# Performance work log

Hardware: AMD Instinct MI355X
Metric: run time of the kernel (lower is better)

## Reference

```python
import jax, jax.numpy as jnp
import numpy as np

N, T, F_IN = 20000, 6, 64   # nodes, seq_len, in_channels
E = 320000                  # edges (avg degree 16)
H, C = 4, 64                # gat1 heads, hidden_channels


def setup_inputs() -> dict:
    key = jax.random.key(0)
    ks = jax.random.split(key, 16)
    p = lambda i, shape, s=0.1: jax.random.normal(ks[i], shape, jnp.float32) * s
    return dict(
        x=p(0, (N, T, F_IN), 1.0),
        edge_index=jax.random.randint(ks[1], (2, E), 0, N),
        # GATv2 layer 1: in=F_IN, out=C per head, H heads, concat
        Wl1=p(2, (F_IN, H * C)), Wr1=p(3, (F_IN, H * C)), att1=p(4, (H, C)), b1=jnp.zeros((H * C,), jnp.float32),
        # GATv2 layer 2: in=H*C, out=C, 1 head, no concat
        Wl2=p(5, (H * C, C)), Wr2=p(6, (H * C, C)), att2=p(7, (1, C)), b2=jnp.zeros((C,), jnp.float32),
        # LSTM (input C, hidden C), pytorch gate order i,f,g,o
        Wih=p(8, (4 * C, C)), Whh=p(9, (4 * C, C)), bih=jnp.zeros((4 * C,), jnp.float32), bhh=jnp.zeros((4 * C,), jnp.float32),
        # MLP head
        Wfc1=p(10, (C, C // 2)), bfc1=jnp.zeros((C // 2,), jnp.float32),
        Wout=p(11, (C // 2, 1)), bout=jnp.zeros((1,), jnp.float32),
    )


def gatv2(xt, src, dst, Wl, Wr, att, bias, n):
    """GATv2Conv (eval mode, no edge_attr): gather -> attn -> segment-softmax -> scatter."""
    heads = att.shape[0]
    d = Wl.shape[1] // heads
    xl = (xt @ Wl).reshape(n, heads, d)   # source transform
    xr = (xt @ Wr).reshape(n, heads, d)   # target transform
    e = jax.nn.leaky_relu(xl[src] + xr[dst], 0.2)           # [E, heads, d]
    logit = jnp.einsum('ehc,hc->eh', e, att)                # [E, heads]
    m = jax.ops.segment_max(logit, dst, num_segments=n)      # per-target max
    ex = jnp.exp(logit - m[dst])
    denom = jax.ops.segment_sum(ex, dst, num_segments=n)
    alpha = ex / denom[dst]                                  # segment softmax
    out = jax.ops.segment_sum(alpha[:, :, None] * xl[src], dst, num_segments=n)
    return out.reshape(n, heads * d) + bias


def reference(x, edge_index, Wl1, Wr1, att1, b1, Wl2, Wr2, att2, b2,
              Wih, Whh, bih, bhh, Wfc1, bfc1, Wout, bout):
    src, dst = edge_index[0], edge_index[1]
    n = x.shape[0]

    def gat_step(carry, xt):                    # per-timestep spatial encoder
        h1 = jax.nn.elu(gatv2(xt, src, dst, Wl1, Wr1, att1, b1, n))
        h2 = jax.nn.elu(gatv2(h1, src, dst, Wl2, Wr2, att2, b2, n))
        return carry, h2

    _, seq = jax.lax.scan(gat_step, 0.0, jnp.swapaxes(x, 0, 1))  # [T, N, C]

    hid = Whh.shape[1]

    def lstm_step(carry, xt):
        h, c = carry
        g = xt @ Wih.T + bih + h @ Whh.T + bhh
        i, f, gg, o = jnp.split(g, 4, axis=-1)
        c = jax.nn.sigmoid(f) * c + jax.nn.sigmoid(i) * jnp.tanh(gg)
        h = jax.nn.sigmoid(o) * jnp.tanh(c)
        return (h, c), None

    h0 = jnp.zeros((n, hid), x.dtype)
    (h_last, _), _ = jax.lax.scan(lstm_step, (h0, h0), seq)

    z = jax.nn.relu(h_last @ Wfc1 + bfc1)
    return z @ Wout + bout
```

## Files before the change

kernel.cpp:

```cpp
#include <hip/hip_runtime.h>
#include <hip/hip_fp16.h>
#include <math.h>

#define N_NODES 20000
#define T_STEPS 6
#define F_INCH  64
#define HC      256
#define CH      64

typedef _Float16 h8    __attribute__((ext_vector_type(8)));
typedef _Float16 hv2   __attribute__((ext_vector_type(2)));
typedef float    f32x4 __attribute__((ext_vector_type(4)));

__device__ __forceinline__ float fast_tanh(float x){
  float e = __expf(2.f*x);
  return 1.f - 2.f/(e + 1.f);
}

__device__ __forceinline__ float fdot2v(hv2 a, hv2 b, float c){
#if __has_builtin(__builtin_amdgcn_fdot2)
  return __builtin_amdgcn_fdot2(a, b, c, false);
#else
  return fmaf((float)a[0], (float)b[0], fmaf((float)a[1], (float)b[1], c));
#endif
}

__device__ __forceinline__ hv2 leaky2(hv2 t){
  hv2 s = t * (_Float16)0.2f;
#if __has_builtin(__builtin_elementwise_max)
  return __builtin_elementwise_max(t, s);
#else
  hv2 r;
  r[0] = (t[0] > s[0]) ? t[0] : s[0];
  r[1] = (t[1] > s[1]) ? t[1] : s[1];
  return r;
#endif
}

__global__ void k_count(const int* __restrict__ dst, int E, int* __restrict__ deg){
  int e = blockIdx.x*256 + threadIdx.x;
  if (e < E) atomicAdd(&deg[dst[e]], 1);
}

__global__ void k_scan(const int* __restrict__ deg, int* __restrict__ row_start, int N){
  __shared__ int wsum[16];
  const int PT = 20;
  int tid = threadIdx.x, wid = tid >> 6, lane = tid & 63;
  int base = tid*PT;
  int loc[PT];
  int s = 0;
  #pragma unroll
  for (int j = 0; j < PT; j++){
    int i = base + j;
    int v = (i < N) ? deg[i] : 0;
    loc[j] = s;
    s += v;
  }
  int ss = s;
  #pragma unroll
  for (int off = 1; off < 64; off <<= 1){
    int t = __shfl_up(ss, off, 64);
    if (lane >= off) ss += t;
  }
  if (lane == 63) wsum[wid] = ss;
  __syncthreads();
  if (tid < 16){
    int w = wsum[tid];
    #pragma unroll
    for (int off = 1; off < 16; off <<= 1){
      int t = __shfl_up(w, off, 64);
      if (tid >= off) w += t;
    }
    wsum[tid] = w;
  }
  __syncthreads();
  int pre = ((wid ? wsum[wid-1] : 0)) + (ss - s);
  #pragma unroll
  for (int j = 0; j < PT; j++){
    int i = base + j;
    if (i < N) row_start[i] = pre + loc[j];
  }
  if (tid == 0) row_start[N] = wsum[15];
}

__global__ void k_scatter(const int* __restrict__ src, const int* __restrict__ dst, int E,
                          const int* __restrict__ row_start, int* __restrict__ cursor,
                          int* __restrict__ csr){
  int e = blockIdx.x*256 + threadIdx.x;
  if (e < E){
    int d = dst[e];
    int pos = atomicAdd(&cursor[d], 1);
    csr[row_start[d] + pos] = src[e];
  }
}

__global__ void k_sort(const int* __restrict__ row_start, int* __restrict__ csr, int N){
  int wid = threadIdx.x >> 6, lane = threadIdx.x & 63;
  int d = blockIdx.x*4 + wid;
  if (d >= N) return;
  int s = row_start[d], e = row_start[d+1], len = e - s;
  if (len <= 1) return;
  if (len <= 64){
    int v = (lane < len) ? csr[s + lane] : 0x7fffffff;
    int rank = 0;
    for (int j = 0; j < len; j++){
      int vj = __shfl(v, j, 64);
      rank += (int)((vj < v) | ((vj == v) & (j < lane)));
    }
    if (lane < len) csr[s + rank] = v;
  } else if (lane == 0){
    for (int i = s+1; i < e; i++){
      int key = csr[i]; int j = i-1;
      while (j >= s && csr[j] > key){ csr[j+1] = csr[j]; j--; }
      csr[j+1] = key;
    }
  }
}

__device__ __forceinline__ void packB_dev(const float* __restrict__ B, _Float16* __restrict__ Bf,
                                          int K, int N, int idx){
  if (idx >= K*N) return;
  int j    = idx & 7;
  int lane = (idx >> 3) & 63;
  int ntk  = idx >> 9;
  int NT = N >> 4;
  int ks = ntk / NT, nt = ntk - ks*NT;
  int k = ks*32 + ((lane >> 4) << 3) + j;
  int n = nt*16 + (lane & 15);
  Bf[idx] = (_Float16)B[k*N + n];
}

__global__ void k_packall(const float* __restrict__ Wih, const float* __restrict__ Whh,
                          const float* __restrict__ bih, const float* __restrict__ bhh,
                          float* __restrict__ Wih4, float* __restrict__ Whh4,
                          float* __restrict__ biasc,
                          const float* __restrict__ Wl1, _Float16* __restrict__ Bl1f,
                          const float* __restrict__ Wr1, _Float16* __restrict__ Br1f,
                          const float* __restrict__ Wl2, _Float16* __restrict__ Bl2f,
                          const float* __restrict__ Wr2, _Float16* __restrict__ Br2f){
  int grp = blockIdx.x >> 6;
  int idx = (blockIdx.x & 63)*256 + threadIdx.x;
  if (grp == 0){
    if (idx < 64*256){
      int k = idx >> 8, cu = idx & 255;
      int u = cu >> 2, g = cu & 3;
      Wih4[idx] = Wih[(g*64+u)*64 + k];
      Whh4[idx] = Whh[(g*64+u)*64 + k];
    }
    if (idx < 256){
      int u = idx >> 2, g = idx & 3;
      biasc[idx] = bih[g*64+u] + bhh[g*64+u];
    }
  } else if (grp == 1){
    packB_dev(Wl1, Bl1f, 64, 256, idx);
  } else if (grp == 2){
    packB_dev(Wr1, Br1f, 64, 256, idx);
  } else if (grp == 3){
    packB_dev(Wl2, Bl2f, 256, 64, idx);
  } else {
    packB_dev(Wr2, Br2f, 256, 64, idx);
  }
}

__global__ __launch_bounds__(256) void k_gemm1_all(
    const float* __restrict__ x, const _Float16* __restrict__ B1f,
    const _Float16* __restrict__ B2f,
    __half* __restrict__ xl_all, __half* __restrict__ xr_all, int M){
  __shared__ _Float16 aT[32*72];
  int t = blockIdx.y;
  const float* A = x + t*F_INCH;
  _Float16* C1 = (_Float16*)(void*)xl_all + (size_t)t*N_NODES*HC;
  _Float16* C2 = (_Float16*)(void*)xr_all + (size_t)t*N_NODES*HC;
  int tid = threadIdx.x;
  int r0 = blockIdx.x*32;
  for (int i = tid; i < 32*64; i += 256){
    int r = i >> 6, k = i & 63;
    int row = r0 + r;
    aT[r*72 + k] = (row < M) ? (_Float16)A[(size_t)row*(T_STEPS*F_INCH) + k] : (_Float16)0.f;
  }
  __syncthreads();
  int wave = tid >> 6, lane = tid & 63;
  int m = wave & 1;
  const h8* Bfrag = (const h8*)((wave >> 1) ? B2f : B1f);
  _Float16* C = (wave >> 1) ? C2 : C1;
  int arow = m*16 + (lane & 15);
  int kb = (lane >> 4) * 8;
  h8 a0 = *(const h8*)&aT[arow*72 + kb];
  h8 a1 = *(const h8*)&aT[arow*72 + 32 + kb];
  f32x4 z = {0.f, 0.f, 0.f, 0.f};
  f32x4 acc[16];
  #pragma unroll
  for (int nt = 0; nt < 16; nt++) acc[nt] = z;
  #pragma unroll
  for (int nt = 0; nt < 16; nt++){
    h8 b0 = Bfrag[nt*64 + lane];
    h8 b1 = Bfrag[(16 + nt)*64 + lane];
    acc[nt] = __builtin_amdgcn_mfma_f32_16x16x32_f16(a0, b0, acc[nt], 0, 0, 0);
    acc[nt] = __builtin_amdgcn_mfma_f32_16x16x32_f16(a1, b1, acc[nt], 0, 0, 0);
  }
  int ccol = lane & 15, crow = (lane >> 4) * 4;
  #pragma unroll
  for (int nt = 0; nt < 16; nt++){
    #pragma unroll
    for (int r = 0; r < 4; r++){
      int row = r0 + m*16 + crow + r;
      if (row < M) C[(size_t)row*256 + nt*16 + ccol] = (_Float16)acc[nt][r];
    }
  }
}

__global__ __launch_bounds__(256) void k_gemm2_all(
    const __half* __restrict__ Aall, const _Float16* __restrict__ B1f,
    const _Float16* __restrict__ B2f,
    __half* __restrict__ C1h_all, __half* __restrict__ C2h_all, int M){
  __shared__ _Float16 aT[32*264];
  int t = blockIdx.y;
  const _Float16* A = (const _Float16*)(const void*)Aall + (size_t)t*N_NODES*HC;
  _Float16* C1 = (_Float16*)(void*)C1h_all + (size_t)t*N_NODES*CH;
  _Float16* C2 = (_Float16*)(void*)C2h_all + (size_t)t*N_NODES*CH;
  int tid = threadIdx.x;
  int r0 = blockIdx.x*32;
  h8 zh = {(_Float16)0.f,(_Float16)0.f,(_Float16)0.f,(_Float16)0.f,
           (_Float16)0.f,(_Float16)0.f,(_Float16)0.f,(_Float16)0.f};
  for (int i = tid; i < 32*32; i += 256){
    int r = i >> 5, c = i & 31;
    int row = r0 + r;
    h8 v = zh;
    if (row < M) v = *(const h8*)&A[(size_t)row*256 + c*8];
    *(h8*)&aT[r*264 + c*8] = v;
  }
  __syncthreads();
  int wave = tid >> 6, lane = tid & 63;
  int m = wave & 1;
  const h8* Bfrag = (const h8*)((wave >> 1) ? B2f : B1f);
  _Float16* C = (wave >> 1) ? C2 : C1;
  int arow = m*16 + (lane & 15);
  int kb = (lane >> 4) * 8;
  f32x4 z = {0.f, 0.f, 0.f, 0.f};
  f32x4 acc[4];
  #pragma unroll
  for (int nt = 0; nt < 4; nt++) acc[nt] = z;
  #pragma unroll
  for (int ks = 0; ks < 8; ks++){
    h8 a = *(const h8*)&aT[arow*264 + ks*32 + kb];
    #pragma unroll
    for (int nt = 0; nt < 4; nt++){
      h8 b = Bfrag[(ks*4 + nt)*64 + lane];
      acc[nt] = __builtin_amdgcn_mfma_f32_16x16x32_f16(a, b, acc[nt], 0, 0, 0);
    }
  }
  int ccol = lane & 15, crow = (lane >> 4) * 4;
  #pragma unroll
  for (int nt = 0; nt < 4; nt++){
    #pragma unroll
    for (int r = 0; r < 4; r++){
      int row = r0 + m*16 + crow + r;
      if (row < M) C[(size_t)row*64 + nt*16 + ccol] = (_Float16)acc[nt][r];
    }
  }
}

__global__ void k_gat1_all(const __half* __restrict__ xl_all, const __half* __restrict__ xr_all,
                           const int* __restrict__ row_start, const int* __restrict__ csr,
                           const float* __restrict__ att, const float* __restrict__ bias,
                           __half* __restrict__ out_all, int N){
  int wid = threadIdx.x >> 6, lane = threadIdx.x & 63;
  int dst = blockIdx.x*4 + wid;
  if (dst >= N) return;
  int t = blockIdx.y;
  const char* xlb = (const char*)(xl_all + (size_t)t*N_NODES*HC);
  const uint2* xrh = (const uint2*)(xr_all + (size_t)t*N_NODES*HC);
  uint2* outh = (uint2*)(out_all + (size_t)t*N_NODES*HC);
  uint2 xr_raw = xrh[(unsigned)(dst*64 + lane)];
  hv2 xr01 = *reinterpret_cast<hv2*>(&xr_raw.x);
  hv2 xr23 = *reinterpret_cast<hv2*>(&xr_raw.y);
  float4 at4 = ((const float4*)att)[lane];
  hv2 at01; at01[0] = (_Float16)at4.x; at01[1] = (_Float16)at4.y;
  hv2 at23; at23[0] = (_Float16)at4.z; at23[1] = (_Float16)at4.w;
  unsigned loff = lane*8u;
  int s0 = __builtin_amdgcn_readfirstlane(row_start[dst]);
  int s1 = __builtin_amdgcn_readfirstlane(row_start[dst+1]);
  float den = 0.f, ax = 0.f, ay = 0.f, az = 0.f, aw = 0.f;

  auto STEP = [&](uint2 raw){
    hv2 h01 = *reinterpret_cast<hv2*>(&raw.x);
    hv2 h23 = *reinterpret_cast<hv2*>(&raw.y);
    hv2 l01 = leaky2(h01 + xr01);
    hv2 l23 = leaky2(h23 + xr23);
    float p = fdot2v(l01, at01, fdot2v(l23, at23, 0.f));
    p += __shfl_xor(p, 1, 64);
    p += __shfl_xor(p, 2, 64);
    p += __shfl_xor(p, 4, 64);
    p += __shfl_xor(p, 8, 64);
    float w = __expf(p);
    den += w;
    ax = fmaf(w, (float)h01[0], ax);
    ay = fmaf(w, (float)h01[1], ay);
    az = fmaf(w, (float)h23[0], az);
    aw = fmaf(w, (float)h23[1], aw);
  };

  for (int base = s0; base < s1; base += 64){
    int rem = s1 - base;
    int cnt = rem < 64 ? rem : 64;
    int idxv = (base + lane < s1) ? csr[base + lane] : 0;
    auto LD = [&](int i)->uint2 {
      int s = __builtin_amdgcn_readlane(idxv, i & 63);
      return *(const uint2*)(xlb + (((size_t)(unsigned)s) << 9) + loff);
    };
    uint2 p0=LD(0), p1=LD(1), p2=LD(2), p3=LD(3);
    uint2 p4=LD(4), p5=LD(5), p6=LD(6), p7=LD(7);
    for (int i = 0; i < cnt; i += 4){
      uint2 n0=LD(i+8), n1=LD(i+9), n2=LD(i+10), n3=LD(i+11);
      if (i + 4 <= cnt){
        STEP(p0); STEP(p1); STEP(p2); STEP(p3);
      } else {
        STEP(p0);
        if (i+1 < cnt) STEP(p1);
        if (i+2 < cnt) STEP(p2);
        if (i+3 < cnt) STEP(p3);
      }
      p0=p4; p1=p5; p2=p6; p3=p7;
      p4=n0; p5=n1; p6=n2; p7=n3;
    }
  }
  float invd = (s1 > s0) ? 1.f/den : 0.f;
  float4 b4 = ((const float4*)bias)[lane];
  float rx = fmaf(ax, invd, b4.x);
  float ry = fmaf(ay, invd, b4.y);
  float rz = fmaf(az, invd, b4.z);
  float rw = fmaf(aw, invd, b4.w);
  rx = rx > 0.f ? rx : (__expf(rx) - 1.f);
  ry = ry > 0.f ? ry : (__expf(ry) - 1.f);
  rz = rz > 0.f ? rz : (__expf(rz) - 1.f);
  rw = rw > 0.f ? rw : (__expf(rw) - 1.f);
  __half2 o01 = __floats2half2_rn(rx, ry);
  __half2 o23 = __floats2half2_rn(rz, rw);
  uint2 o;
  o.x = *reinterpret_cast<unsigned int*>(&o01);
  o.y = *reinterpret_cast<unsigned int*>(&o23);
  outh[(unsigned)(dst*64 + lane)] = o;
}

__global__ void k_gat2_all(const __half* __restrict__ xl_all, const __half* __restrict__ xr_all,
                           const int* __restrict__ row_start, const int* __restrict__ csr,
                           const float* __restrict__ att, const float* __restrict__ bias,
                           __half* __restrict__ out_all, int N){
  int wid = threadIdx.x >> 6, lane = threadIdx.x & 63;
  int dst = blockIdx.x*4 + wid;
  if (dst >= N) return;
  int t = blockIdx.y;
  int g = lane >> 4, q = lane & 15;
  const char* xlb = (const char*)(xl_all + (size_t)t*N_NODES*CH);
  const uint2* xrh = (const uint2*)(xr_all + (size_t)t*N_NODES*CH);
  uint2* outh = (uint2*)(out_all + (size_t)t*N_NODES*CH);
  uint2 xr_raw = xrh[(unsigned)(dst*16 + q)];
  hv2 xr01 = *reinterpret_cast<hv2*>(&xr_raw.x);
  hv2 xr23 = *reinterpret_cast<hv2*>(&xr_raw.y);
  float4 at4 = ((const float4*)att)[q];
  hv2 at01; at01[0] = (_Float16)at4.x; at01[1] = (_Float16)at4.y;
  hv2 at23; at23[0] = (_Float16)at4.z; at23[1] = (_Float16)at4.w;
  unsigned qoff = q*8u;
  int s0 = __builtin_amdgcn_readfirstlane(row_start[dst]);
  int s1 = __builtin_amdgcn_readfirstlane(row_start[dst+1]);
  float den = 0.f, ax = 0.f, ay = 0.f, az = 0.f, aw = 0.f;

  for (int base = s0; base < s1; base += 64){
    int rem = s1 - base;
    int cnt = rem < 64 ? rem : 64;
    int idxv = (base + lane < s1) ? csr[base + lane] : 0;
    int K = (cnt + 3) >> 2;
    int e0 = g, e1 = g + 4;
    int sA = __shfl(idxv, e0 < cnt ? e0 : 0, 64);
    int sB = __shfl(idxv, e1 < cnt ? e1 : 0, 64);
    uint2 vA = *(const uint2*)(xlb + (((size_t)(unsigned)sA) << 7) + qoff);
    uint2 vB = *(const uint2*)(xlb + (((size_t)(unsigned)sB) << 7) + qoff);
    for (int k = 0; k < K; k++){
      int en = 4*k + 8 + g;
      int sN = __shfl(idxv, en < cnt ? en : 0, 64);
      uint2 vN = *(const uint2*)(xlb + (((size_t)(unsigned)sN) << 7) + qoff);
      int e = 4*k + g;
      if (e < cnt){
        hv2 h01 = *reinterpret_cast<hv2*>(&vA.x);
        hv2 h23 = *reinterpret_cast<hv2*>(&vA.y);
        hv2 l01 = leaky2(h01 + xr01);
        hv2 l23 = leaky2(h23 + xr23);
        float p = fdot2v(l01, at01, fdot2v(l23, at23, 0.f));
        p += __shfl_xor(p, 1, 64);
        p += __shfl_xor(p, 2, 64);
        p += __shfl_xor(p, 4, 64);
        p += __shfl_xor(p, 8, 64);
        float w = __expf(p);
        den += w;
        ax = fmaf(w, (float)h01[0], ax);
        ay = fmaf(w, (float)h01[1], ay);
        az = fmaf(w, (float)h23[0], az);
        aw = fmaf(w, (float)h23[1], aw);
      }
      vA = vB; vB = vN;
    }
  }
  den += __shfl_xor(den, 16, 64); den += __shfl_xor(den, 32, 64);
  ax  += __shfl_xor(ax, 16, 64);  ax  += __shfl_xor(ax, 32, 64);
  ay  += __shfl_xor(ay, 16, 64);  ay  += __shfl_xor(ay, 32, 64);
  az  += __shfl_xor(az, 16, 64);  az  += __shfl_xor(az, 32, 64);
  aw  += __shfl_xor(aw, 16, 64);  aw  += __shfl_xor(aw, 32, 64);
  float invd = (s1 > s0) ? 1.f/den : 0.f;
  float4 b4 = ((const float4*)bias)[q];
  float rx = fmaf(ax, invd, b4.x);
  float ry = fmaf(ay, invd, b4.y);
  float rz = fmaf(az, invd, b4.z);
  float rw = fmaf(aw, invd, b4.w);
  rx = rx > 0.f ? rx : (__expf(rx) - 1.f);
  ry = ry > 0.f ? ry : (__expf(ry) - 1.f);
  rz = rz > 0.f ? rz : (__expf(rz) - 1.f);
  rw = rw > 0.f ? rw : (__expf(rw) - 1.f);
  if (g == 0){
    __half2 o01 = __floats2half2_rn(rx, ry);
    __half2 o23 = __floats2half2_rn(rz, rw);
    uint2 o;
    o.x = *reinterpret_cast<unsigned int*>(&o01);
    o.y = *reinterpret_cast<unsigned int*>(&o23);
    outh[(unsigned)(dst*16 + q)] = o;
  }
}

__global__ __launch_bounds__(256) void k_lstm_mlp(
    const __half* __restrict__ h2f_all,
    const float* __restrict__ Wih4, const float* __restrict__ Whh4,
    const float* __restrict__ biasc,
    const float* __restrict__ Wfc1, const float* __restrict__ bfc1,
    const float* __restrict__ Wout, const float* __restrict__ bout,
    float* __restrict__ out, int N){
  __shared__ float WiS[8*256];
  __shared__ float WhS[8*256];
  __shared__ float xT[64*20];
  __shared__ float hT[64*20];
  int tid = threadIdx.x;
  int u = tid & 63, rq = tid >> 6;
  int r0 = blockIdx.x*16;
  for (int idx = tid; idx < 64*20; idx += 256) hT[idx] = 0.f;
  float4 bc = ((const float4*)biasc)[u];
  const float4* Wi4 = (const float4*)Wih4;
  const float4* Wh4 = (const float4*)Whh4;
  float4* WiS4 = (float4*)WiS;
  float4* WhS4 = (float4*)WhS;
  const float4* xT4 = (const float4*)xT;
  const float4* hT4 = (const float4*)hT;
  float c[4] = {0,0,0,0};
  float h[4] = {0,0,0,0};
  for (int t = 0; t < T_STEPS; t++){
    const __half* xt = h2f_all + (size_t)t*N_NODES*CH;
    for (int idx = tid; idx < 16*64; idx += 256){
      int r = idx >> 6, k = idx & 63;
      int row = r0 + r;
      xT[k*20 + r] = (row < N) ? __half2float(xt[(size_t)row*64 + k]) : 0.f;
    }
    float ai[4], af[4], ag[4], ao[4];
    #pragma unroll
    for (int j = 0; j < 4; j++){ ai[j]=bc.x; af[j]=bc.y; ag[j]=bc.z; ao[j]=bc.w; }
    for (int s = 0; s < 8; s++){
      __syncthreads();
      WiS4[tid]     = Wi4[s*512 + tid];
      WiS4[tid+256] = Wi4[s*512 + tid + 256];
      WhS4[tid]     = Wh4[s*512 + tid];
      WhS4[tid+256] = Wh4[s*512 + tid + 256];
      __syncthreads();
      #pragma unroll
      for (int kk = 0; kk < 8; kk++){
        int k = s*8 + kk;
        float4 wi = WiS4[kk*64 + u];
        float4 wh = WhS4[kk*64 + u];
        float4 xq = xT4[k*5 + rq];
        float4 hq = hT4[k*5 + rq];
        float xv[4] = {xq.x, xq.y, xq.z, xq.w};
        float hv[4] = {hq.x, hq.y, hq.z, hq.w};
        #pragma unroll
        for (int j = 0; j < 4; j++){
          ai[j] = fmaf(xv[j], wi.x, ai[j]); ai[j] = fmaf(hv[j], wh.x, ai[j]);
          af[j] = fmaf(xv[j], wi.y, af[j]); af[j] = fmaf(hv[j], wh.y, af[j]);
          ag[j] = fmaf(xv[j], wi.z, ag[j]); ag[j] = fmaf(hv[j], wh.z, ag[j]);
          ao[j] = fmaf(xv[j], wi.w, ao[j]); ao[j] = fmaf(hv[j], wh.w, ao[j]);
        }
      }
    }
    #pragma unroll
    for (int j = 0; j < 4; j++){
      float I = 1.f/(1.f + __expf(-ai[j]));
      float F = 1.f/(1.f + __expf(-af[j]));
      float O = 1.f/(1.f + __expf(-ao[j]));
      float G = fast_tanh(ag[j]);
      c[j] = fmaf(F, c[j], I*G);
      h[j] = O * fast_tanh(c[j]);
    }
    __syncthreads();
    #pragma unroll
    for (int j = 0; j < 4; j++) hT[u*20 + rq*4 + j] = h[j];
  }
  __syncthreads();
  int row_l = tid >> 4;
  int jj = (tid & 15) * 2;
  int row = r0 + row_l;
  float acc0 = bfc1[jj], acc1 = bfc1[jj+1];
  #pragma unroll 8
  for (int k = 0; k < 64; k++){
    float hv = hT[k*20 + row_l];
    acc0 = fmaf(hv, Wfc1[k*32 + jj],   acc0);
    acc1 = fmaf(hv, Wfc1[k*32 + jj+1], acc1);
  }
  acc0 = fmaxf(acc0, 0.f) * Wout[jj];
  acc1 = fmaxf(acc1, 0.f) * Wout[jj+1];
  float v = acc0 + acc1;
  v += __shfl_xor(v, 1, 64);
  v += __shfl_xor(v, 2, 64);
  v += __shfl_xor(v, 4, 64);
  v += __shfl_xor(v, 8, 64);
  if ((tid & 15) == 0 && row < N) out[row] = v + bout[0];
}

extern "C" void kernel_launch(void* const* d_in, const int* in_sizes, int n_in,
                              void* d_out, int out_size, void* d_ws, size_t ws_size,
                              hipStream_t stream){
  const float* x    = (const float*)d_in[0];
  const int*   edge = (const int*)  d_in[1];
  const float* Wl1  = (const float*)d_in[2];
  const float* Wr1  = (const float*)d_in[3];
  const float* att1 = (const float*)d_in[4];
  const float* b1   = (const float*)d_in[5];
  const float* Wl2  = (const float*)d_in[6];
  const float* Wr2  = (const float*)d_in[7];
  const float* att2 = (const float*)d_in[8];
  const float* b2   = (const float*)d_in[9];
  const float* Wih  = (const float*)d_in[10];
  const float* Whh  = (const float*)d_in[11];
  const float* bih  = (const float*)d_in[12];
  const float* bhh  = (const float*)d_in[13];
  const float* Wfc1 = (const float*)d_in[14];
  const float* bfc1 = (const float*)d_in[15];
  const float* Wout = (const float*)d_in[16];
  const float* bout = (const float*)d_in[17];
  float* out = (float*)d_out;

  const int N = N_NODES;
  const int E = in_sizes[1] / 2;

  char* p = (char*)d_ws;
  auto alloc = [&](size_t bytes)->char*{ char* q = p; p += (bytes + 255) & ~(size_t)255; return q; };
  int* csr       = (int*)alloc((size_t)E*sizeof(int));
  int* row_start = (int*)alloc((size_t)(N+1)*sizeof(int));
  int* deg       = (int*)alloc((size_t)N*sizeof(int));
  int* cursor    = (int*)alloc((size_t)N*sizeof(int));
  const size_t NB = (size_t)T_STEPS*N_NODES*HC;
  char* bufA = alloc(NB*2);
  char* bufB = alloc(NB*2);
  char* bufC = alloc(NB*2);
  float* Wih4   = (float*)alloc(64*256*4);
  float* Whh4   = (float*)alloc(64*256*4);
  float* biasc  = (float*)alloc(256*4);
  _Float16* Bl1f = (_Float16*)alloc(64*256*2);
  _Float16* Br1f = (_Float16*)alloc(64*256*2);
  _Float16* Bl2f = (_Float16*)alloc(256*64*2);
  _Float16* Br2f = (_Float16*)alloc(256*64*2);

  __half* xl1h_all = (__half*)bufA;
  __half* xr1h_all = (__half*)bufB;
  __half* h1_all   = (__half*)bufC;
  __half* xl2h_all = (__half*)bufA;
  __half* xr2h_all = (__half*)(bufA + (size_t)T_STEPS*N_NODES*CH*2);
  __half* h2f_all  = (__half*)bufB;

  const int* srcIdx = edge;
  const int* dstIdx = edge + E;

  hipMemsetAsync(deg, 0, (size_t)((char*)cursor - (char*)deg) + (size_t)N*4, stream);

  k_count  <<<(E+255)/256, 256, 0, stream>>>(dstIdx, E, deg);
  k_scan   <<<1, 1024, 0, stream>>>(deg, row_start, N);
  k_scatter<<<(E+255)/256, 256, 0, stream>>>(srcIdx, dstIdx, E, row_start, cursor, csr);
  k_sort   <<<(N+3)/4, 256, 0, stream>>>(row_start, csr, N);
  k_packall<<<320, 256, 0, stream>>>(Wih, Whh, bih, bhh, Wih4, Whh4, biasc,
                                     Wl1, Bl1f, Wr1, Br1f, Wl2, Bl2f, Wr2, Br2f);

  dim3 gGemm((N+31)/32, T_STEPS);
  dim3 gGat ((N+3)/4,  T_STEPS);
  k_gemm1_all<<<gGemm, 256, 0, stream>>>(x, Bl1f, Br1f, xl1h_all, xr1h_all, N);
  k_gat1_all <<<gGat,  256, 0, stream>>>(xl1h_all, xr1h_all, row_start, csr, att1, b1, h1_all, N);
  k_gemm2_all<<<gGemm, 256, 0, stream>>>(h1_all, Bl2f, Br2f, xl2h_all, xr2h_all, N);
  k_gat2_all <<<gGat,  256, 0, stream>>>(xl2h_all, xr2h_all, row_start, csr, att2, b2, h2f_all, N);

  k_lstm_mlp<<<(N+15)/16, 256, 0, stream>>>(h2f_all, Wih4, Whh4, biasc,
                                            Wfc1, bfc1, Wout, bout, out, N);
}
```

Baseline: 475.1 us.

## Split LSTM into batched MFMA input-gate GEMM and MFMA recurrent kernel

Replaces the fp32 scalar-FMA LSTM kernel with two kernels. The first precomputes input-gate projections for all timesteps as one batched fp16 MFMA GEMM with fused bias. The second runs the recurrence with one wave per 16 rows, using MFMA for h@Whh and adding the precomputed gates, followed by the MLP head. This trades the shared-memory-heavy scalar loop for matrix cores, at the cost of an extra fp16 gates buffer round-trip through memory and fp16 rounding of h and the gates.

Measured after the change: 403.3 us (median of 2 runs). 1.18x faster.

```diff
diff --git a/kernel.cpp b/kernel.cpp
--- a/kernel.cpp
+++ b/kernel.cpp
@@ -130,35 +130,43 @@
   Bf[idx] = (_Float16)B[k*N + n];
 }
 
-__global__ void k_packall(const float* __restrict__ Wih, const float* __restrict__ Whh,
-                          const float* __restrict__ bih, const float* __restrict__ bhh,
-                          float* __restrict__ Wih4, float* __restrict__ Whh4,
+__device__ __forceinline__ void packBT_dev(const float* __restrict__ W, _Float16* __restrict__ Bf,
+                                           int K, int N, int idx){
+  if (idx >= K*N) return;
+  int j    = idx & 7;
+  int lane = (idx >> 3) & 63;
+  int ntk  = idx >> 9;
+  int NT = N >> 4;
+  int ks = ntk / NT, nt = ntk - ks*NT;
+  int k = ks*32 + ((lane >> 4) << 3) + j;
+  int n = nt*16 + (lane & 15);
+  Bf[idx] = (_Float16)W[n*K + k];
+}
+
+__global__ void k_packall(const float* __restrict__ bih, const float* __restrict__ bhh,
                           float* __restrict__ biasc,
                           const float* __restrict__ Wl1, _Float16* __restrict__ Bl1f,
                           const float* __restrict__ Wr1, _Float16* __restrict__ Br1f,
                           const float* __restrict__ Wl2, _Float16* __restrict__ Bl2f,
-                          const float* __restrict__ Wr2, _Float16* __restrict__ Br2f){
+                          const float* __restrict__ Wr2, _Float16* __restrict__ Br2f,
+                          const float* __restrict__ Wih, _Float16* __restrict__ Wihf,
+                          const float* __restrict__ Whh, _Float16* __restrict__ Whhf){
   int grp = blockIdx.x >> 6;
   int idx = (blockIdx.x & 63)*256 + threadIdx.x;
   if (grp == 0){
-    if (idx < 64*256){
-      int k = idx >> 8, cu = idx & 255;
-      int u = cu >> 2, g = cu & 3;
-      Wih4[idx] = Wih[(g*64+u)*64 + k];
-      Whh4[idx] = Whh[(g*64+u)*64 + k];
-    }
-    if (idx < 256){
-      int u = idx >> 2, g = idx & 3;
-      biasc[idx] = bih[g*64+u] + bhh[g*64+u];
-    }
+    if (idx < 256) biasc[idx] = bih[idx] + bhh[idx];
   } else if (grp == 1){
     packB_dev(Wl1, Bl1f, 64, 256, idx);
   } else if (grp == 2){
     packB_dev(Wr1, Br1f, 64, 256, idx);
   } else if (grp == 3){
     packB_dev(Wl2, Bl2f, 256, 64, idx);
+  } else if (grp == 4){
+    packB_dev(Wr2, Br2f, 256, 64, idx);
+  } else if (grp == 5){
+    packBT_dev(Wih, Wihf, 64, 256, idx);
   } else {
-    packB_dev(Wr2, Br2f, 256, 64, idx);
+    packBT_dev(Whh, Whhf, 64, 256, idx);
   }
 }
 
@@ -425,97 +433,123 @@
   }
 }
 
-__global__ __launch_bounds__(256) void k_lstm_mlp(
-    const __half* __restrict__ h2f_all,
-    const float* __restrict__ Wih4, const float* __restrict__ Whh4,
-    const float* __restrict__ biasc,
+__global__ __launch_bounds__(256) void k_gemmx_all(
+    const __half* __restrict__ Aall, const _Float16* __restrict__ Bf,
+    const float* __restrict__ biasc, __half* __restrict__ Call){
+  __shared__ _Float16 aT[32*72];
+  int tid = threadIdx.x;
+  int r0 = blockIdx.x*32;
+  {
+    int r = tid >> 3, c8 = tid & 7;
+    *(h8*)&aT[r*72 + c8*8] =
+        *(const h8*)&((const _Float16*)(const void*)Aall)[((size_t)(r0+r))*64 + c8*8];
+  }
+  __syncthreads();
+  int wave = tid >> 6, lane = tid & 63;
+  int m = wave & 1, nh = wave >> 1;
+  int arow = m*16 + (lane & 15);
+  int kb = (lane >> 4) * 8;
+  h8 a0 = *(const h8*)&aT[arow*72 + kb];
+  h8 a1 = *(const h8*)&aT[arow*72 + 32 + kb];
+  const h8* B = (const h8*)Bf;
+  f32x4 z = {0.f, 0.f, 0.f, 0.f};
+  f32x4 acc[8];
+  #pragma unroll
+  for (int nt = 0; nt < 8; nt++) acc[nt] = z;
+  #pragma unroll
+  for (int nt = 0; nt < 8; nt++){
+    int ntg = nh*8 + nt;
+    acc[nt] = __builtin_amdgcn_mfma_f32_16x16x32_f16(a0, B[ntg*64 + lane],        acc[nt], 0,0,0);
+    acc[nt] = __builtin_amdgcn_mfma_f32_16x16x32_f16(a1, B[(16 + ntg)*64 + lane], acc[nt], 0,0,0);
+  }
+  int ccol = lane & 15, crow = (lane >> 4) * 4;
+  _Float16* C = (_Float16*)(void*)Call;
+  #pragma unroll
+  for (int nt = 0; nt < 8; nt++){
+    int ntg = nh*8 + nt;
+    int col = ntg*16 + ccol;
+    float b = biasc[col];
+    #pragma unroll
+    for (int r = 0; r < 4; r++){
+      C[(size_t)(r0 + m*16 + crow + r)*256 + col] = (_Float16)(acc[nt][r] + b);
+    }
+  }
+}
+
+__global__ __launch_bounds__(64) void k_lstm_rec(
+    const __half* __restrict__ gatesx,
+    const _Float16* __restrict__ Whhf,
     const float* __restrict__ Wfc1, const float* __restrict__ bfc1,
     const float* __restrict__ Wout, const float* __restrict__ bout,
     float* __restrict__ out, int N){
-  __shared__ float WiS[8*256];
-  __shared__ float WhS[8*256];
-  __shared__ float xT[64*20];
-  __shared__ float hT[64*20];
-  int tid = threadIdx.x;
-  int u = tid & 63, rq = tid >> 6;
+  __shared__ _Float16 gxT[16*264];
+  __shared__ _Float16 hT[16*68];
+  int lane = threadIdx.x;
   int r0 = blockIdx.x*16;
-  for (int idx = tid; idx < 64*20; idx += 256) hT[idx] = 0.f;
-  float4 bc = ((const float4*)biasc)[u];
-  const float4* Wi4 = (const float4*)Wih4;
-  const float4* Wh4 = (const float4*)Whh4;
-  float4* WiS4 = (float4*)WiS;
-  float4* WhS4 = (float4*)WhS;
-  const float4* xT4 = (const float4*)xT;
-  const float4* hT4 = (const float4*)hT;
-  float c[4] = {0,0,0,0};
-  float h[4] = {0,0,0,0};
+  for (int i = lane; i < 16*68; i += 64) hT[i] = (_Float16)0.f;
+  int ccol = lane & 15, crow = (lane >> 4) * 4;
+  int arow_off = (lane & 15)*68 + ((lane >> 4) << 3);
+  const h8* Bfrag = (const h8*)Whhf;
+  const _Float16* gxb = (const _Float16*)(const void*)gatesx;
+  float c[16];
+  #pragma unroll
+  for (int i = 0; i < 16; i++) c[i] = 0.f;
+
   for (int t = 0; t < T_STEPS; t++){
-    const __half* xt = h2f_all + (size_t)t*N_NODES*CH;
-    for (int idx = tid; idx < 16*64; idx += 256){
-      int r = idx >> 6, k = idx & 63;
-      int row = r0 + r;
-      xT[k*20 + r] = (row < N) ? __half2float(xt[(size_t)row*64 + k]) : 0.f;
-    }
-    float ai[4], af[4], ag[4], ao[4];
-    #pragma unroll
-    for (int j = 0; j < 4; j++){ ai[j]=bc.x; af[j]=bc.y; ag[j]=bc.z; ao[j]=bc.w; }
-    for (int s = 0; s < 8; s++){
-      __syncthreads();
-      WiS4[tid]     = Wi4[s*512 + tid];
-      WiS4[tid+256] = Wi4[s*512 + tid + 256];
-      WhS4[tid]     = Wh4[s*512 + tid];
-      WhS4[tid+256] = Wh4[s*512 + tid + 256];
-      __syncthreads();
+    const _Float16* gx = gxb + ((size_t)t*N_NODES + r0)*256;
+    #pragma unroll
+    for (int it = 0; it < 8; it++){
+      int idx = it*64 + lane;
+      int r = idx >> 5, c8 = idx & 31;
+      *(h8*)&gxT[r*264 + c8*8] = *(const h8*)&gx[(size_t)r*256 + c8*8];
+    }
+    h8 a0 = *(const h8*)&hT[arow_off];
+    h8 a1 = *(const h8*)&hT[arow_off + 32];
+    f32x4 z = {0.f, 0.f, 0.f, 0.f};
+    f32x4 acc[16];
+    #pragma unroll
+    for (int nt = 0; nt < 16; nt++) acc[nt] = z;
+    #pragma unroll
+    for (int nt = 0; nt < 16; nt++){
+      acc[nt] = __builtin_amdgcn_mfma_f32_16x16x32_f16(a0, Bfrag[nt*64 + lane],        acc[nt], 0,0,0);
+      acc[nt] = __builtin_amdgcn_mfma_f32_16x16x32_f16(a1, Bfrag[(16 + nt)*64 + lane], acc[nt], 0,0,0);
+    }
+    #pragma unroll
+    for (int us = 0; us < 4; us++){
+      int ucol = us*16 + ccol;
       #pragma unroll
-      for (int kk = 0; kk < 8; kk++){
-        int k = s*8 + kk;
-        float4 wi = WiS4[kk*64 + u];
-        float4 wh = WhS4[kk*64 + u];
-        float4 xq = xT4[k*5 + rq];
-        float4 hq = hT4[k*5 + rq];
-        float xv[4] = {xq.x, xq.y, xq.z, xq.w};
-        float hv[4] = {hq.x, hq.y, hq.z, hq.w};
-        #pragma unroll
-        for (int j = 0; j < 4; j++){
-          ai[j] = fmaf(xv[j], wi.x, ai[j]); ai[j] = fmaf(hv[j], wh.x, ai[j]);
-          af[j] = fmaf(xv[j], wi.y, af[j]); af[j] = fmaf(hv[j], wh.y, af[j]);
-          ag[j] = fmaf(xv[j], wi.z, ag[j]); ag[j] = fmaf(hv[j], wh.z, ag[j]);
-          ao[j] = fmaf(xv[j], wi.w, ao[j]); ao[j] = fmaf(hv[j], wh.w, ao[j]);
-        }
+      for (int r = 0; r < 4; r++){
+        int row = crow + r;
+        float gi = acc[us     ][r] + (float)gxT[row*264 +       ucol];
+        float gf = acc[4  + us][r] + (float)gxT[row*264 +  64 + ucol];
+        float gg = acc[8  + us][r] + (float)gxT[row*264 + 128 + ucol];
+        float go = acc[12 + us][r] + (float)gxT[row*264 + 192 + ucol];
+        float I = 1.f/(1.f + __expf(-gi));
+        float F = 1.f/(1.f + __expf(-gf));
+        float O = 1.f/(1.f + __expf(-go));
+        float G = fast_tanh(gg);
+        float cc = fmaf(F, c[us*4 + r], I*G);
+        c[us*4 + r] = cc;
+        hT[row*68 + ucol] = (_Float16)(O * fast_tanh(cc));
       }
     }
-    #pragma unroll
-    for (int j = 0; j < 4; j++){
-      float I = 1.f/(1.f + __expf(-ai[j]));
-      float F = 1.f/(1.f + __expf(-af[j]));
-      float O = 1.f/(1.f + __expf(-ao[j]));
-      float G = fast_tanh(ag[j]);
-      c[j] = fmaf(F, c[j], I*G);
-      h[j] = O * fast_tanh(c[j]);
-    }
-    __syncthreads();
-    #pragma unroll
-    for (int j = 0; j < 4; j++) hT[u*20 + rq*4 + j] = h[j];
-  }
-  __syncthreads();
-  int row_l = tid >> 4;
-  int jj = (tid & 15) * 2;
-  int row = r0 + row_l;
-  float acc0 = bfc1[jj], acc1 = bfc1[jj+1];
-  #pragma unroll 8
+  }
+  int rowm = lane >> 2;
+  int cb = (lane & 3) * 8;
+  float a8[8];
+  #pragma unroll
+  for (int j = 0; j < 8; j++) a8[j] = bfc1[cb + j];
   for (int k = 0; k < 64; k++){
-    float hv = hT[k*20 + row_l];
-    acc0 = fmaf(hv, Wfc1[k*32 + jj],   acc0);
-    acc1 = fmaf(hv, Wfc1[k*32 + jj+1], acc1);
-  }
-  acc0 = fmaxf(acc0, 0.f) * Wout[jj];
-  acc1 = fmaxf(acc1, 0.f) * Wout[jj+1];
-  float v = acc0 + acc1;
+    float hv = (float)hT[rowm*68 + k];
+    #pragma unroll
+    for (int j = 0; j < 8; j++) a8[j] = fmaf(hv, Wfc1[k*32 + cb + j], a8[j]);
+  }
+  float v = 0.f;
+  #pragma unroll
+  for (int j = 0; j < 8; j++) v += fmaxf(a8[j], 0.f) * Wout[cb + j];
   v += __shfl_xor(v, 1, 64);
   v += __shfl_xor(v, 2, 64);
-  v += __shfl_xor(v, 4, 64);
-  v += __shfl_xor(v, 8, 64);
-  if ((tid & 15) == 0 && row < N) out[row] = v + bout[0];
+  if ((lane & 3) == 0) out[r0 + rowm] = v + bout[0];
 }
 
 extern "C" void kernel_launch(void* const* d_in, const int* in_sizes, int n_in,
@@ -554,13 +588,13 @@
   char* bufA = alloc(NB*2);
   char* bufB = alloc(NB*2);
   char* bufC = alloc(NB*2);
-  float* Wih4   = (float*)alloc(64*256*4);
-  float* Whh4   = (float*)alloc(64*256*4);
   float* biasc  = (float*)alloc(256*4);
   _Float16* Bl1f = (_Float16*)alloc(64*256*2);
   _Float16* Br1f = (_Float16*)alloc(64*256*2);
   _Float16* Bl2f = (_Float16*)alloc(256*64*2);
   _Float16* Br2f = (_Float16*)alloc(256*64*2);
+  _Float16* Wihf = (_Float16*)alloc(64*256*2);
+  _Float16* Whhf = (_Float16*)alloc(64*256*2);
 
   __half* xl1h_all = (__half*)bufA;
   __half* xr1h_all = (__half*)bufB;
@@ -568,6 +602,7 @@
   __half* xl2h_all = (__half*)bufA;
   __half* xr2h_all = (__half*)(bufA + (size_t)T_STEPS*N_NODES*CH*2);
   __half* h2f_all  = (__half*)bufB;
+  __half* gatesx   = (__half*)bufC;
 
   const int* srcIdx = edge;
   const int* dstIdx = edge + E;
@@ -578,8 +613,9 @@
   k_scan   <<<1, 1024, 0, stream>>>(deg, row_start, N);
   k_scatter<<<(E+255)/256, 256, 0, stream>>>(srcIdx, dstIdx, E, row_start, cursor, csr);
   k_sort   <<<(N+3)/4, 256, 0, stream>>>(row_start, csr, N);
-  k_packall<<<320, 256, 0, stream>>>(Wih, Whh, bih, bhh, Wih4, Whh4, biasc,
-                                     Wl1, Bl1f, Wr1, Br1f, Wl2, Bl2f, Wr2, Br2f);
+  k_packall<<<448, 256, 0, stream>>>(bih, bhh, biasc,
+                                     Wl1, Bl1f, Wr1, Br1f, Wl2, Bl2f, Wr2, Br2f,
+                                     Wih, Wihf, Whh, Whhf);
 
   dim3 gGemm((N+31)/32, T_STEPS);
   dim3 gGat ((N+3)/4,  T_STEPS);
@@ -588,6 +624,6 @@
   k_gemm2_all<<<gGemm, 256, 0, stream>>>(h1_all, Bl2f, Br2f, xl2h_all, xr2h_all, N);
   k_gat2_all <<<gGat,  256, 0, stream>>>(xl2h_all, xr2h_all, row_start, csr, att2, b2, h2f_all, N);
 
-  k_lstm_mlp<<<(N+15)/16, 256, 0, stream>>>(h2f_all, Wih4, Whh4, biasc,
-                                            Wfc1, bfc1, Wout, bout, out, N);
-}
+  k_gemmx_all<<<(T_STEPS*N)/32, 256, 0, stream>>>(h2f_all, Wihf, biasc, gatesx);
+  k_lstm_rec <<<N/16, 64, 0, stream>>>(gatesx, Whhf, Wfc1, bfc1, Wout, bout, out, N);
+}
```
